# Kernel tuning notes

Hardware: AMD Instinct MI355X
Metric: run time of the kernel (lower is better)

The kernel has to match this reference:

```python
import jax, jax.numpy as jnp
import numpy as np

K_TOP = 2  # n_experts_per_tok
W_SCALE = 0.02  # keep activations numerically tame


def setup_inputs() -> dict:
    key = jax.random.key(0)
    ks = jax.random.split(key, 8)
    D, F, E = 1024, 1024, 8
    B, T = 4, 2048
    x = jax.random.normal(ks[0], (B, T, D), dtype=jnp.float32)
    router_w = jax.random.normal(ks[1], (D, E), dtype=jnp.float32) * W_SCALE
    sg = jax.random.normal(ks[2], (D, F), dtype=jnp.float32) * W_SCALE
    su = jax.random.normal(ks[3], (D, F), dtype=jnp.float32) * W_SCALE
    sd = jax.random.normal(ks[4], (F, D), dtype=jnp.float32) * W_SCALE
    wg = jax.random.normal(ks[5], (E, D, F), dtype=jnp.float32) * W_SCALE
    wu = jax.random.normal(ks[6], (E, D, F), dtype=jnp.float32) * W_SCALE
    wd = jax.random.normal(ks[7], (E, F, D), dtype=jnp.float32) * W_SCALE
    return {"x": x, "router_w": router_w, "sg": sg, "su": su, "sd": sd,
            "wg": wg, "wu": wu, "wd": wd}


def reference(x, router_w, sg, su, sd, wg, wu, wd):
    B, T, D = x.shape
    E = wg.shape[0]
    flat = x.reshape(-1, D)                       # [N, D]
    N = flat.shape[0]

    # shared SwiGLU expert (n_shared_experts = 1)
    shared = (jax.nn.silu(flat @ sg) * (flat @ su)) @ sd  # [N, D]

    # top-k softmax router with renormalization
    probs = jax.nn.softmax(flat @ router_w, axis=-1)      # [N, E]
    topk_p, topk_i = jax.lax.top_k(probs, K_TOP)          # [N, K]
    topk_p = topk_p / (jnp.sum(topk_p, axis=-1, keepdims=True) + 1e-9)

    # dense combine weights: scatter renormalized probs into [N, E]
    cw = jnp.zeros((N, E), dtype=flat.dtype).at[
        jnp.arange(N)[:, None], topk_i].add(topk_p)

    # per-expert SwiGLU on all tokens, weighted combine (jit-friendly MoE form)
    h = jax.nn.silu(jnp.einsum('nd,edf->nef', flat, wg)) \
        * jnp.einsum('nd,edf->nef', flat, wu)             # [N, E, F]
    eo = jnp.einsum('nef,efd->ned', h, wd)                # [N, E, D]
    routed = jnp.einsum('ned,ne->nd', eo, cw)             # [N, D]

    return (shared + routed).reshape(B, T, D)
```

## Files before the change

kernel.cpp:

```cpp
#include <hip/hip_runtime.h>

#define N_TOK    8192
#define D_DIM    1024
#define F_DIM    1024
#define NESH     9
#define MAX_RTD  18432
#define MAX_ROWS 26624
#define BT 128
#define BK 32
#define NK 32
#define BM2 256
#define BK2 64
#define NK2 16

#define MO 16
#define MT 25

typedef float  f4    __attribute__((ext_vector_type(4)));
typedef float  f32x4 __attribute__((ext_vector_type(4)));
typedef short  s16x8 __attribute__((ext_vector_type(8)));
typedef unsigned short u16x8 __attribute__((ext_vector_type(8)));
typedef unsigned short u16x4 __attribute__((ext_vector_type(4)));

static __device__ __forceinline__ unsigned short f2bf(float f) {
    union { float f; unsigned u; } v; v.f = f;
    unsigned r = v.u + 0x7FFFu + ((v.u >> 16) & 1u);
    return (unsigned short)(r >> 16);
}
static __device__ __forceinline__ float bf2f(unsigned short u) {
    union { unsigned u; float f; } v; v.u = ((unsigned)u) << 16; return v.f;
}

#define GLDS(gp, lp) __builtin_amdgcn_global_load_lds( \
    (const __attribute__((address_space(1))) void*)(gp), \
    (__attribute__((address_space(3))) void*)(lp), 16, 0, 0)

#define RSWZ64(row, idx) ((idx) ^ (((row) & 7) << 3))

__global__ __launch_bounds__(256) void k_transpose(
    const float* __restrict__ wg, const float* __restrict__ wu,
    const float* __restrict__ wd, const float* __restrict__ sg,
    const float* __restrict__ su, const float* __restrict__ sd,
    unsigned short* __restrict__ wgt, unsigned short* __restrict__ wut,
    unsigned short* __restrict__ wdt)
{
    int bx = blockIdx.x;
    int m = bx >> 8;
    int tile = bx & 255;
    int ty = tile >> 4, tx = tile & 15;
    int set = m / 9, e = m % 9;
    const float* src; unsigned short* dst;
    if (set == 0)      { src = (e < 8) ? wg + (size_t)e*1048576 : sg; dst = wgt + (size_t)e*1048576; }
    else if (set == 1) { src = (e < 8) ? wu + (size_t)e*1048576 : su; dst = wut + (size_t)e*1048576; }
    else               { src = (e < 8) ? wd + (size_t)e*1048576 : sd; dst = wdt + (size_t)e*1048576; }

    __shared__ unsigned short ts[64 * 67];
    int t = threadIdx.x;
    int rT0 = ty * 64, cT0 = tx * 64;
    #pragma unroll
    for (int i = 0; i < 4; i++) {
        int idx = t + i * 256;
        int a  = idx >> 4;
        int b4 = (idx & 15) * 4;
        f4 v = *(const f4*)(src + (size_t)(cT0 + a) * 1024 + rT0 + b4);
        ts[a * 67 + b4 + 0] = f2bf(v[0]);
        ts[a * 67 + b4 + 1] = f2bf(v[1]);
        ts[a * 67 + b4 + 2] = f2bf(v[2]);
        ts[a * 67 + b4 + 3] = f2bf(v[3]);
    }
    __syncthreads();
    #pragma unroll
    for (int i = 0; i < 2; i++) {
        int slot = t + i * 256;
        int r  = slot >> 3;
        int c8 = (slot & 7) * 8;
        u16x8 o;
        #pragma unroll
        for (int k = 0; k < 8; k++) o[k] = ts[(c8 + k) * 67 + r];
        *(u16x8*)&dst[(size_t)(rT0 + r) * 1024 + cT0 + c8] = o;
    }
}

__global__ __launch_bounds__(256) void k_router(
    const float* __restrict__ x, const float* __restrict__ rw,
    unsigned short* __restrict__ xb,
    int* __restrict__ tk_i, float* __restrict__ tk_w)
{
    int wid = threadIdx.x >> 6, lane = threadIdx.x & 63;
    int n = blockIdx.x * 4 + wid;
    const float* xr = x + (size_t)n * D_DIM;
    unsigned short* xbr = xb + (size_t)n * D_DIM;
    float acc[8] = {0,0,0,0,0,0,0,0};
    #pragma unroll
    for (int it = 0; it < 4; it++) {
        int d0 = it * 256 + lane * 4;
        f4 xv = *(const f4*)(xr + d0);
        #pragma unroll
        for (int j = 0; j < 4; j++) {
            f4 r0 = *(const f4*)(rw + (size_t)(d0 + j) * 8);
            f4 r1 = *(const f4*)(rw + (size_t)(d0 + j) * 8 + 4);
            acc[0] += xv[j]*r0[0]; acc[1] += xv[j]*r0[1]; acc[2] += xv[j]*r0[2]; acc[3] += xv[j]*r0[3];
            acc[4] += xv[j]*r1[0]; acc[5] += xv[j]*r1[1]; acc[6] += xv[j]*r1[2]; acc[7] += xv[j]*r1[3];
        }
        u16x4 o; o[0]=f2bf(xv[0]); o[1]=f2bf(xv[1]); o[2]=f2bf(xv[2]); o[3]=f2bf(xv[3]);
        *(u16x4*)&xbr[d0] = o;
    }
    #pragma unroll
    for (int e = 0; e < 8; e++)
        for (int off = 32; off; off >>= 1)
            acc[e] += __shfl_xor(acc[e], off, 64);
    if (lane == 0) {
        float mx = acc[0];
        for (int e = 1; e < 8; e++) mx = fmaxf(mx, acc[e]);
        float p[8], s = 0.f;
        for (int e = 0; e < 8; e++) { p[e] = expf(acc[e] - mx); s += p[e]; }
        int i0 = 0;
        for (int e = 1; e < 8; e++) if (p[e] > p[i0]) i0 = e;
        int i1 = (i0 == 0) ? 1 : 0;
        for (int e = 0; e < 8; e++) if (e != i0 && p[e] > p[i1]) i1 = e;
        float p0 = p[i0] / s, p1 = p[i1] / s;
        float rs = p0 + p1 + 1e-9f;
        tk_i[2*n] = i0;  tk_i[2*n+1] = i1;
        tk_w[2*n] = p0 / rs;  tk_w[2*n+1] = p1 / rs;
    }
}

__global__ __launch_bounds__(1024) void k_count_scatter(
    const int* __restrict__ tk_i, const float* __restrict__ tk_w,
    int* __restrict__ meta,
    int* __restrict__ row_token, int* __restrict__ row_expert,
    int* __restrict__ tok_pos)
{
    __shared__ int cnt[1024 * 9];
    __shared__ int tot[8];
    __shared__ int off[9];
    const int t = threadIdx.x;
    const int lane = t & 63;
    const int wid = t >> 6;

    #pragma unroll
    for (int e = 0; e < 8; e++) cnt[t * 9 + e] = 0;
    __syncthreads();

    #pragma unroll
    for (int j = 0; j < 8; j++) {
        int n = t * 8 + j;
        cnt[t * 9 + tk_i[2 * n]]++;
        cnt[t * 9 + tk_i[2 * n + 1]]++;
    }
    __syncthreads();

    if (wid < 8) {
        const int e = wid;
        int carry = 0;
        for (int c = 0; c < 16; c++) {
            int i = c * 64 + lane;
            int v = cnt[i * 9 + e];
            int s = v;
            #pragma unroll
            for (int d = 1; d < 64; d <<= 1) {
                int u = __shfl_up(s, d, 64);
                if (lane >= d) s += u;
            }
            cnt[i * 9 + e] = s - v + carry;
            carry += __shfl(s, 63, 64);
        }
        if (lane == 0) tot[e] = carry;
    }
    __syncthreads();

    if (t == 0) {
        int acc = 0;
        #pragma unroll
        for (int e = 0; e < 8; e++) {
            off[e] = acc;
            meta[MO + e] = acc;
            acc += ((tot[e] + 255) >> 8) << 8;
        }
        off[8] = acc;
        meta[MO + 8] = acc;
        meta[MT] = acc + N_TOK;
    }
    __syncthreads();

    #pragma unroll
    for (int j = 0; j < 8; j++) {
        int n = t * 8 + j;
        #pragma unroll
        for (int k = 0; k < 2; k++) {
            int e = tk_i[2 * n + k];
            int pos = off[e] + cnt[t * 9 + e];
            cnt[t * 9 + e] = cnt[t * 9 + e] + 1;
            row_token[pos] = n; row_expert[pos] = e;
            tok_pos[2 * n + k] = pos;
        }
        int ps = off[8] + n;
        row_token[ps] = n; row_expert[ps] = 8;
    }
    #pragma unroll
    for (int e = 0; e < 8; e++) {
        int start = off[e] + tot[e], end = off[e + 1];
        for (int i = start + t; i < end; i += 1024) {
            row_token[i] = -1;
            row_expert[i] = e;
        }
    }
}

__global__ __launch_bounds__(512, 4) void k_gemm1(
    const unsigned short* __restrict__ xb,
    const unsigned short* __restrict__ wgt,
    const unsigned short* __restrict__ wut,
    const int* __restrict__ row_token,
    const int* __restrict__ row_expert,
    const int* __restrict__ meta,
    unsigned short* __restrict__ h)
{
    const int total = meta[MT];
    const int orig = blockIdx.x;
    const int bid = (orig & 7) * 208 + (orig >> 3);
    const int rt = bid >> 3, ct = bid & 7;
    const int row0 = rt * BT;
    if (row0 >= total) return;
    const int e = row_expert[row0];

    __shared__ __align__(16) unsigned short sA[2 * 128 * 32];
    __shared__ __align__(16) unsigned short sBg[2 * 128 * 32];
    __shared__ __align__(16) unsigned short sBu[2 * 128 * 32];

    const int t = threadIdx.x;
    const int lane = t & 63;
    const int lr = lane & 15;
    const int kl = lane >> 4;
    const int wid = t >> 6;
    const int wr = wid >> 2, wc = wid & 3;

    const int srow = t >> 2;
    const int scg  = (t & 3) ^ ((srow >> 1) & 3);
    int tok = row_token[row0 + srow];
    if (tok < 0) tok = 0;
    const unsigned short* srcA = xb + (size_t)tok * D_DIM + scg * 8;
    const unsigned short* srcG = wgt + ((size_t)e * F_DIM + ct * BT + srow) * D_DIM + scg * 8;
    const unsigned short* srcU = wut + ((size_t)e * F_DIM + ct * BT + srow) * D_DIM + scg * 8;

    f32x4 accg[4][2] = {}, accu[4][2] = {};

#define ST1(bb, k0) do { \
    GLDS(srcA + (k0), &sA[(bb) * 4096 + t * 8]); \
    GLDS(srcG + (k0), &sBg[(bb) * 4096 + t * 8]); \
    GLDS(srcU + (k0), &sBu[(bb) * 4096 + t * 8]); } while (0)

#define COMPUTE1(bb) do { \
    const unsigned short* pA  = &sA[(bb) * 4096]; \
    const unsigned short* pG  = &sBg[(bb) * 4096]; \
    const unsigned short* pU  = &sBu[(bb) * 4096]; \
    s16x8 a_[4], g_[2], q_[2]; \
    _Pragma("unroll") \
    for (int m_ = 0; m_ < 4; m_++) { \
        int row = wr * 64 + m_ * 16 + lr; \
        a_[m_] = *(const s16x8*)&pA[row * 32 + ((kl ^ ((row >> 1) & 3)) << 3)]; } \
    _Pragma("unroll") \
    for (int n_ = 0; n_ < 2; n_++) { \
        int row = wc * 32 + n_ * 16 + lr; \
        int ix = row * 32 + ((kl ^ ((row >> 1) & 3)) << 3); \
        g_[n_] = *(const s16x8*)&pG[ix]; \
        q_[n_] = *(const s16x8*)&pU[ix]; } \
    _Pragma("unroll") \
    for (int m_ = 0; m_ < 4; m_++) \
        _Pragma("unroll") \
        for (int n_ = 0; n_ < 2; n_++) { \
            accg[m_][n_] = __builtin_amdgcn_mfma_f32_16x16x32_bf16(a_[m_], g_[n_], accg[m_][n_], 0, 0, 0); \
            accu[m_][n_] = __builtin_amdgcn_mfma_f32_16x16x32_bf16(a_[m_], q_[n_], accu[m_][n_], 0, 0, 0); } \
    } while (0)

    ST1(0, 0);
    for (int u = 0; u < NK; u++) {
        if (u < NK - 1) {
            ST1((u + 1) & 1, (u + 1) * BK);
            asm volatile("s_waitcnt vmcnt(3)" ::: "memory");
        } else {
            asm volatile("s_waitcnt vmcnt(0)" ::: "memory");
        }
        __builtin_amdgcn_s_barrier();
        __builtin_amdgcn_s_setprio(1);
        COMPUTE1(u & 1);
        __builtin_amdgcn_s_setprio(0);
        asm volatile("" ::: "memory");
        __builtin_amdgcn_s_barrier();
    }

    #pragma unroll
    for (int m = 0; m < 4; m++)
        #pragma unroll
        for (int r = 0; r < 4; r++) {
            int grow = row0 + wr * 64 + m * 16 + (lane >> 4) * 4 + r;
            unsigned short* hrow = h + (size_t)grow * F_DIM + ct * BT + wc * 32 + lr;
            #pragma unroll
            for (int n = 0; n < 2; n++) {
                float g = accg[m][n][r], uu = accu[m][n][r];
                float sv = g / (1.f + __expf(-g));
                hrow[n * 16] = f2bf(sv * uu);
            }
        }
#undef ST1
#undef COMPUTE1
}

__global__ __launch_bounds__(512, 2) void k_gemm2(
    const unsigned short* __restrict__ h,
    const unsigned short* __restrict__ wdt,
    const int* __restrict__ row_expert,
    const int* __restrict__ meta,
    unsigned short* __restrict__ eo,
    float* __restrict__ out)
{
    const int total = meta[MT];
    const int off8 = meta[MO + 8];
    const int orig = blockIdx.x;
    const int bid = (orig & 7) * 52 + (orig >> 3);
    const int rt = bid >> 2, ct = bid & 3;
    const int row0 = rt * BM2;
    if (row0 >= total) return;
    const int e = row_expert[row0];

    __shared__ __align__(16) unsigned short sA[2 * BM2 * BK2];
    __shared__ __align__(16) unsigned short sB[2 * BM2 * BK2];

    const int t = threadIdx.x;
    const int lane = t & 63;
    const int lr = lane & 15;
    const int wid = t >> 6;
    const int wr = wid >> 2, wc = wid & 3;

    const unsigned short* asrc[4];
    const unsigned short* bsrc[4];
    #pragma unroll
    for (int i = 0; i < 4; i++) {
        int slot = t + i * 512;
        int row = slot >> 3;
        int cg  = (slot & 7) ^ (row & 7);
        asrc[i] = h + (size_t)(row0 + row) * F_DIM + cg * 8;
        bsrc[i] = wdt + ((size_t)e * D_DIM + ct * 256 + row) * F_DIM + cg * 8;
    }

    f32x4 acc[8][4] = {};

#define STAGE_A2(bb, k0) do { \
    unsigned short* dA = &sA[(bb) * (BM2 * BK2)]; \
    _Pragma("unroll") \
    for (int i_ = 0; i_ < 4; i_++) GLDS(asrc[i_] + (k0), &dA[(t + i_ * 512) * 8]); \
    } while (0)
#define STAGE_B2(bb, k0) do { \
    unsigned short* dB = &sB[(bb) * (BM2 * BK2)]; \
    _Pragma("unroll") \
    for (int i_ = 0; i_ < 4; i_++) GLDS(bsrc[i_] + (k0), &dB[(t + i_ * 512) * 8]); \
    } while (0)

#define COMPUTE2(bb) do { \
    const unsigned short* pA = &sA[(bb) * (BM2 * BK2)]; \
    const unsigned short* pB = &sB[(bb) * (BM2 * BK2)]; \
    _Pragma("unroll") \
    for (int kk = 0; kk < BK2; kk += 32) { \
        const int koff = kk + (lane >> 4) * 8; \
        s16x8 a_[8], b_[4]; \
        _Pragma("unroll") \
        for (int m_ = 0; m_ < 8; m_++) { \
            int row = wr * 128 + m_ * 16 + lr; \
            a_[m_] = *(const s16x8*)&pA[RSWZ64(row, row * BK2 + koff)]; } \
        _Pragma("unroll") \
        for (int n_ = 0; n_ < 4; n_++) { \
            int row = wc * 64 + n_ * 16 + lr; \
            b_[n_] = *(const s16x8*)&pB[RSWZ64(row, row * BK2 + koff)]; } \
        _Pragma("unroll") \
        for (int m_ = 0; m_ < 8; m_++) \
            _Pragma("unroll") \
            for (int n_ = 0; n_ < 4; n_++) \
                acc[m_][n_] = __builtin_amdgcn_mfma_f32_16x16x32_bf16(a_[m_], b_[n_], acc[m_][n_], 0, 0, 0); \
    } } while (0)

    STAGE_A2(0, 0);
    STAGE_B2(0, 0);
    for (int u = 0; u < NK2; u++) {
        if (u < NK2 - 1) {
            STAGE_A2((u + 1) & 1, (u + 1) * BK2);
            STAGE_B2((u + 1) & 1, (u + 1) * BK2);
            asm volatile("s_waitcnt vmcnt(8)" ::: "memory");
        } else {
            asm volatile("s_waitcnt vmcnt(0)" ::: "memory");
        }
        __builtin_amdgcn_s_barrier();
        __builtin_amdgcn_s_setprio(1);
        COMPUTE2(u & 1);
        __builtin_amdgcn_s_setprio(0);
        asm volatile("" ::: "memory");
        __builtin_amdgcn_s_barrier();
    }

    if (e < 8) {
        #pragma unroll
        for (int mf = 0; mf < 8; mf++)
            #pragma unroll
            for (int r = 0; r < 4; r++) {
                int grow = row0 + wr * 128 + mf * 16 + (lane >> 4) * 4 + r;
                unsigned short* erow = eo + (size_t)grow * D_DIM + ct * 256 + wc * 64 + lr;
                #pragma unroll
                for (int ni = 0; ni < 4; ni++)
                    erow[ni * 16] = f2bf(acc[mf][ni][r]);
            }
    } else {
        #pragma unroll
        for (int mf = 0; mf < 8; mf++)
            #pragma unroll
            for (int r = 0; r < 4; r++) {
                int grow = row0 + wr * 128 + mf * 16 + (lane >> 4) * 4 + r;
                int tok = grow - off8;
                float* orow = out + (size_t)tok * D_DIM + ct * 256 + wc * 64 + lr;
                #pragma unroll
                for (int ni = 0; ni < 4; ni++)
                    orow[ni * 16] = acc[mf][ni][r];
            }
    }
#undef STAGE_A2
#undef STAGE_B2
#undef COMPUTE2
}

__global__ __launch_bounds__(256) void k_combine(
    const unsigned short* __restrict__ eo,
    const int* __restrict__ tok_pos, const float* __restrict__ tk_w,
    float* __restrict__ out)
{
    const int t = threadIdx.x;
    const int n = blockIdx.x * 2 + (t >> 7);
    const int c0 = (t & 127) * 8;
    const int p0 = tok_pos[2 * n], p1 = tok_pos[2 * n + 1];
    const float w0 = tk_w[2 * n], w1 = tk_w[2 * n + 1];
    u16x8 a = *(const u16x8*)&eo[(size_t)p0 * D_DIM + c0];
    u16x8 b = *(const u16x8*)&eo[(size_t)p1 * D_DIM + c0];
    float* orow = out + (size_t)n * D_DIM + c0;
    f4 o0 = *(f4*)orow, o1 = *(f4*)(orow + 4);
    #pragma unroll
    for (int j = 0; j < 4; j++) {
        o0[j] += w0 * bf2f(a[j])     + w1 * bf2f(b[j]);
        o1[j] += w0 * bf2f(a[4 + j]) + w1 * bf2f(b[4 + j]);
    }
    *(f4*)orow = o0;
    *(f4*)(orow + 4) = o1;
}

extern "C" void kernel_launch(void* const* d_in, const int* in_sizes, int n_in,
                              void* d_out, int out_size, void* d_ws, size_t ws_size,
                              hipStream_t stream)
{
    const float* x  = (const float*)d_in[0];
    const float* rw = (const float*)d_in[1];
    const float* sg = (const float*)d_in[2];
    const float* su = (const float*)d_in[3];
    const float* sd = (const float*)d_in[4];
    const float* wg = (const float*)d_in[5];
    const float* wu = (const float*)d_in[6];
    const float* wd = (const float*)d_in[7];
    float* out = (float*)d_out;

    char* p = (char*)d_ws;
    unsigned short* xb  = (unsigned short*)p; p += (size_t)N_TOK * D_DIM * 2;
    unsigned short* wgt = (unsigned short*)p; p += (size_t)NESH * D_DIM * F_DIM * 2;
    unsigned short* wut = (unsigned short*)p; p += (size_t)NESH * D_DIM * F_DIM * 2;
    unsigned short* wdt = (unsigned short*)p; p += (size_t)NESH * D_DIM * F_DIM * 2;
    unsigned short* h   = (unsigned short*)p; p += (size_t)MAX_ROWS * F_DIM * 2;
    int*   row_token  = (int*)p;   p += (size_t)MAX_ROWS * 4;
    int*   row_expert = (int*)p;   p += (size_t)MAX_ROWS * 4;
    int*   tok_pos = (int*)p;      p += (size_t)N_TOK * 2 * 4;
    int*   tk_i = (int*)p;         p += (size_t)N_TOK * 2 * 4;
    float* tk_w = (float*)p;       p += (size_t)N_TOK * 2 * 4;
    int*   meta = (int*)p;         p += 1024;
    if ((size_t)(p - (char*)d_ws) > ws_size) return;

    unsigned short* eo = wgt;

    k_router<<<N_TOK / 4, 256, 0, stream>>>(x, rw, xb, tk_i, tk_w);
    k_transpose<<<27 * 256, 256, 0, stream>>>(wg, wu, wd, sg, su, sd, wgt, wut, wdt);
    k_count_scatter<<<1, 1024, 0, stream>>>(tk_i, tk_w, meta, row_token, row_expert, tok_pos);
    k_gemm1<<<(MAX_ROWS / BT) * 8, 512, 0, stream>>>(xb, wgt, wut, row_token, row_expert, meta, h);
    k_gemm2<<<(MAX_ROWS / BM2) * 4, 512, 0, stream>>>(h, wdt, row_expert, meta, eo, out);
    k_combine<<<N_TOK / 2, 256, 0, stream>>>(eo, tok_pos, tk_w, out);
}
```

Measured before the change: 320.9 us.

## Halve gemm2 K-tile, split x conversion out of router, rework transpose LDS

The down-projection GEMM now uses a 32-wide K tile with twice as many iterations and a new XOR swizzle. This halves its shared memory footprint so more blocks may fit per CU, but it pays for more barriers per tile. The bf16 conversion of x moves from the router into a separate vectorized kernel, and the router now reads scalar floats per lane. The weight transpose now loads scalars, writes transposed into a padded LDS tile, and stores 16-byte rows, trading wide global reads for simpler LDS access.

```diff
diff --git a/kernel.cpp b/kernel.cpp
--- a/kernel.cpp
+++ b/kernel.cpp
@@ -10,8 +10,8 @@
 #define BK 32
 #define NK 32
 #define BM2 256
-#define BK2 64
-#define NK2 16
+#define BK2 32
+#define NK2 32
 
 #define MO 16
 #define MT 25
@@ -20,7 +20,6 @@
 typedef float  f32x4 __attribute__((ext_vector_type(4)));
 typedef short  s16x8 __attribute__((ext_vector_type(8)));
 typedef unsigned short u16x8 __attribute__((ext_vector_type(8)));
-typedef unsigned short u16x4 __attribute__((ext_vector_type(4)));
 
 static __device__ __forceinline__ unsigned short f2bf(float f) {
     union { float f; unsigned u; } v; v.f = f;
@@ -35,7 +34,17 @@
     (const __attribute__((address_space(1))) void*)(gp), \
     (__attribute__((address_space(3))) void*)(lp), 16, 0, 0)
 
-#define RSWZ64(row, idx) ((idx) ^ (((row) & 7) << 3))
+__global__ __launch_bounds__(256) void k_convert_x(
+    const float* __restrict__ x, unsigned short* __restrict__ xb)
+{
+    int g = blockIdx.x * 256 + threadIdx.x;
+    const f4* xs = (const f4*)x;
+    f4 a = xs[2*g], b = xs[2*g+1];
+    u16x8 o;
+    o[0]=f2bf(a[0]); o[1]=f2bf(a[1]); o[2]=f2bf(a[2]); o[3]=f2bf(a[3]);
+    o[4]=f2bf(b[0]); o[5]=f2bf(b[1]); o[6]=f2bf(b[2]); o[7]=f2bf(b[3]);
+    *(u16x8*)&xb[8*(size_t)g] = o;
+}
 
 __global__ __launch_bounds__(256) void k_transpose(
     const float* __restrict__ wg, const float* __restrict__ wu,
@@ -54,56 +63,41 @@
     else if (set == 1) { src = (e < 8) ? wu + (size_t)e*1048576 : su; dst = wut + (size_t)e*1048576; }
     else               { src = (e < 8) ? wd + (size_t)e*1048576 : sd; dst = wdt + (size_t)e*1048576; }
 
-    __shared__ unsigned short ts[64 * 67];
+    __shared__ __align__(16) unsigned short ts[64 * 80];
     int t = threadIdx.x;
     int rT0 = ty * 64, cT0 = tx * 64;
     #pragma unroll
-    for (int i = 0; i < 4; i++) {
-        int idx = t + i * 256;
-        int a  = idx >> 4;
-        int b4 = (idx & 15) * 4;
-        f4 v = *(const f4*)(src + (size_t)(cT0 + a) * 1024 + rT0 + b4);
-        ts[a * 67 + b4 + 0] = f2bf(v[0]);
-        ts[a * 67 + b4 + 1] = f2bf(v[1]);
-        ts[a * 67 + b4 + 2] = f2bf(v[2]);
-        ts[a * 67 + b4 + 3] = f2bf(v[3]);
+    for (int i = 0; i < 16; i++) {
+        int lin = t + i * 256;
+        int mr = lin >> 6, mc = lin & 63;
+        float v = src[(size_t)(cT0 + mr) * 1024 + rT0 + mc];
+        ts[mc * 80 + mr] = f2bf(v);
     }
     __syncthreads();
     #pragma unroll
     for (int i = 0; i < 2; i++) {
-        int slot = t + i * 256;
-        int r  = slot >> 3;
-        int c8 = (slot & 7) * 8;
-        u16x8 o;
-        #pragma unroll
-        for (int k = 0; k < 8; k++) o[k] = ts[(c8 + k) * 67 + r];
-        *(u16x8*)&dst[(size_t)(rT0 + r) * 1024 + cT0 + c8] = o;
+        int r = (t >> 3) + i * 32;
+        int c0 = (t & 7) * 8;
+        *(u16x8*)&dst[(size_t)(rT0 + r) * 1024 + cT0 + c0] = *(u16x8*)&ts[r * 80 + c0];
     }
 }
 
 __global__ __launch_bounds__(256) void k_router(
     const float* __restrict__ x, const float* __restrict__ rw,
-    unsigned short* __restrict__ xb,
     int* __restrict__ tk_i, float* __restrict__ tk_w)
 {
     int wid = threadIdx.x >> 6, lane = threadIdx.x & 63;
     int n = blockIdx.x * 4 + wid;
     const float* xr = x + (size_t)n * D_DIM;
-    unsigned short* xbr = xb + (size_t)n * D_DIM;
     float acc[8] = {0,0,0,0,0,0,0,0};
     #pragma unroll
-    for (int it = 0; it < 4; it++) {
-        int d0 = it * 256 + lane * 4;
-        f4 xv = *(const f4*)(xr + d0);
-        #pragma unroll
-        for (int j = 0; j < 4; j++) {
-            f4 r0 = *(const f4*)(rw + (size_t)(d0 + j) * 8);
-            f4 r1 = *(const f4*)(rw + (size_t)(d0 + j) * 8 + 4);
-            acc[0] += xv[j]*r0[0]; acc[1] += xv[j]*r0[1]; acc[2] += xv[j]*r0[2]; acc[3] += xv[j]*r0[3];
-            acc[4] += xv[j]*r1[0]; acc[5] += xv[j]*r1[1]; acc[6] += xv[j]*r1[2]; acc[7] += xv[j]*r1[3];
-        }
-        u16x4 o; o[0]=f2bf(xv[0]); o[1]=f2bf(xv[1]); o[2]=f2bf(xv[2]); o[3]=f2bf(xv[3]);
-        *(u16x4*)&xbr[d0] = o;
+    for (int it = 0; it < 16; it++) {
+        int d = it * 64 + lane;
+        float xv = xr[d];
+        f4 r0 = *(const f4*)(rw + (size_t)d * 8);
+        f4 r1 = *(const f4*)(rw + (size_t)d * 8 + 4);
+        acc[0] += xv * r0[0]; acc[1] += xv * r0[1]; acc[2] += xv * r0[2]; acc[3] += xv * r0[3];
+        acc[4] += xv * r1[0]; acc[5] += xv * r1[1]; acc[6] += xv * r1[2]; acc[7] += xv * r1[3];
     }
     #pragma unroll
     for (int e = 0; e < 8; e++)
@@ -329,62 +323,53 @@
     const int t = threadIdx.x;
     const int lane = t & 63;
     const int lr = lane & 15;
+    const int kl = lane >> 4;
     const int wid = t >> 6;
     const int wr = wid >> 2, wc = wid & 3;
 
-    const unsigned short* asrc[4];
-    const unsigned short* bsrc[4];
-    #pragma unroll
-    for (int i = 0; i < 4; i++) {
+    const unsigned short* asrc[2];
+    const unsigned short* bsrc[2];
+    #pragma unroll
+    for (int i = 0; i < 2; i++) {
         int slot = t + i * 512;
-        int row = slot >> 3;
-        int cg  = (slot & 7) ^ (row & 7);
+        int row = slot >> 2;
+        int cg  = (slot & 3) ^ ((row >> 1) & 3);
         asrc[i] = h + (size_t)(row0 + row) * F_DIM + cg * 8;
         bsrc[i] = wdt + ((size_t)e * D_DIM + ct * 256 + row) * F_DIM + cg * 8;
     }
 
     f32x4 acc[8][4] = {};
 
-#define STAGE_A2(bb, k0) do { \
-    unsigned short* dA = &sA[(bb) * (BM2 * BK2)]; \
-    _Pragma("unroll") \
-    for (int i_ = 0; i_ < 4; i_++) GLDS(asrc[i_] + (k0), &dA[(t + i_ * 512) * 8]); \
+#define ST2(bb, k0) do { \
+    GLDS(asrc[0] + (k0), &sA[(bb) * 8192 + t * 8]); \
+    GLDS(asrc[1] + (k0), &sA[(bb) * 8192 + (t + 512) * 8]); \
+    GLDS(bsrc[0] + (k0), &sB[(bb) * 8192 + t * 8]); \
+    GLDS(bsrc[1] + (k0), &sB[(bb) * 8192 + (t + 512) * 8]); } while (0)
+
+#define COMPUTE2(bb) do { \
+    const unsigned short* pA = &sA[(bb) * 8192]; \
+    const unsigned short* pB = &sB[(bb) * 8192]; \
+    s16x8 a_[8], b_[4]; \
+    _Pragma("unroll") \
+    for (int m_ = 0; m_ < 8; m_++) { \
+        int row = wr * 128 + m_ * 16 + lr; \
+        a_[m_] = *(const s16x8*)&pA[row * 32 + ((kl ^ ((row >> 1) & 3)) << 3)]; } \
+    _Pragma("unroll") \
+    for (int n_ = 0; n_ < 4; n_++) { \
+        int row = wc * 64 + n_ * 16 + lr; \
+        b_[n_] = *(const s16x8*)&pB[row * 32 + ((kl ^ ((row >> 1) & 3)) << 3)]; } \
+    _Pragma("unroll") \
+    for (int m_ = 0; m_ < 8; m_++) \
+        _Pragma("unroll") \
+        for (int n_ = 0; n_ < 4; n_++) \
+            acc[m_][n_] = __builtin_amdgcn_mfma_f32_16x16x32_bf16(a_[m_], b_[n_], acc[m_][n_], 0, 0, 0); \
     } while (0)
-#define STAGE_B2(bb, k0) do { \
-    unsigned short* dB = &sB[(bb) * (BM2 * BK2)]; \
-    _Pragma("unroll") \
-    for (int i_ = 0; i_ < 4; i_++) GLDS(bsrc[i_] + (k0), &dB[(t + i_ * 512) * 8]); \
-    } while (0)
-
-#define COMPUTE2(bb) do { \
-    const unsigned short* pA = &sA[(bb) * (BM2 * BK2)]; \
-    const unsigned short* pB = &sB[(bb) * (BM2 * BK2)]; \
-    _Pragma("unroll") \
-    for (int kk = 0; kk < BK2; kk += 32) { \
-        const int koff = kk + (lane >> 4) * 8; \
-        s16x8 a_[8], b_[4]; \
-        _Pragma("unroll") \
-        for (int m_ = 0; m_ < 8; m_++) { \
-            int row = wr * 128 + m_ * 16 + lr; \
-            a_[m_] = *(const s16x8*)&pA[RSWZ64(row, row * BK2 + koff)]; } \
-        _Pragma("unroll") \
-        for (int n_ = 0; n_ < 4; n_++) { \
-            int row = wc * 64 + n_ * 16 + lr; \
-            b_[n_] = *(const s16x8*)&pB[RSWZ64(row, row * BK2 + koff)]; } \
-        _Pragma("unroll") \
-        for (int m_ = 0; m_ < 8; m_++) \
-            _Pragma("unroll") \
-            for (int n_ = 0; n_ < 4; n_++) \
-                acc[m_][n_] = __builtin_amdgcn_mfma_f32_16x16x32_bf16(a_[m_], b_[n_], acc[m_][n_], 0, 0, 0); \
-    } } while (0)
-
-    STAGE_A2(0, 0);
-    STAGE_B2(0, 0);
+
+    ST2(0, 0);
     for (int u = 0; u < NK2; u++) {
         if (u < NK2 - 1) {
-            STAGE_A2((u + 1) & 1, (u + 1) * BK2);
-            STAGE_B2((u + 1) & 1, (u + 1) * BK2);
-            asm volatile("s_waitcnt vmcnt(8)" ::: "memory");
+            ST2((u + 1) & 1, (u + 1) * BK2);
+            asm volatile("s_waitcnt vmcnt(4)" ::: "memory");
         } else {
             asm volatile("s_waitcnt vmcnt(0)" ::: "memory");
         }
@@ -420,8 +405,7 @@
                     orow[ni * 16] = acc[mf][ni][r];
             }
     }
-#undef STAGE_A2
-#undef STAGE_B2
+#undef ST2
 #undef COMPUTE2
 }
 
@@ -478,8 +462,9 @@
 
     unsigned short* eo = wgt;
 
-    k_router<<<N_TOK / 4, 256, 0, stream>>>(x, rw, xb, tk_i, tk_w);
+    k_convert_x<<<N_TOK * D_DIM / 8 / 256, 256, 0, stream>>>(x, xb);
     k_transpose<<<27 * 256, 256, 0, stream>>>(wg, wu, wd, sg, su, sd, wgt, wut, wdt);
+    k_router<<<N_TOK / 4, 256, 0, stream>>>(x, rw, tk_i, tk_w);
     k_count_scatter<<<1, 1024, 0, stream>>>(tk_i, tk_w, meta, row_token, row_expert, tok_pos);
     k_gemm1<<<(MAX_ROWS / BT) * 8, 512, 0, stream>>>(xb, wgt, wut, row_token, row_expert, meta, h);
     k_gemm2<<<(MAX_ROWS / BM2) * 4, 512, 0, stream>>>(h, wdt, row_expert, meta, eo, out);
```

New measurement: 321.2 us. No clear change (+0.1%).
